# Kernel optimization log

Hardware: AMD Instinct MI355X
Metric: run time of the kernel (lower is better)

Reference implementation:

```python
import jax, jax.numpy as jnp
import numpy as np

N = 50000
E = 800000
D_IN = 128
D_H = 128
N_CLASSES = 40
N_HIDDEN = 2


def _gcn_norm(edge_index, num_nodes):
    # Add self loops, compute symmetric normalization D^-1/2 (A+I) D^-1/2
    loops = jnp.arange(num_nodes, dtype=edge_index.dtype)
    src = jnp.concatenate([edge_index[0], loops])
    dst = jnp.concatenate([edge_index[1], loops])
    deg = jax.ops.segment_sum(jnp.ones_like(src, dtype=jnp.float32), dst,
                              num_segments=num_nodes)
    dinv = jnp.where(deg > 0, jax.lax.rsqrt(jnp.maximum(deg, 1.0)), 0.0)
    norm = dinv[src] * dinv[dst]  # [E+N]
    return src, dst, norm


def _gcn_conv(x, src, dst, norm, W, b):
    h = x @ W                          # [N, d_out] transform first (PyG order)
    msg = h[src] * norm[:, None]       # gather + scale, [E+N, d_out]
    out = jax.ops.segment_sum(msg, dst, num_segments=x.shape[0])
    return out + b


def setup_inputs() -> dict:
    key = jax.random.key(0)
    ks = jax.random.split(key, 8)
    x = jax.random.normal(ks[0], (N, D_IN), dtype=jnp.float32)
    edge_index = jax.random.randint(ks[1], (2, E), 0, N, dtype=jnp.int64)
    s = 1.0 / np.sqrt(D_IN)
    W1 = jax.random.uniform(ks[2], (D_IN, D_H), minval=-s, maxval=s, dtype=jnp.float32)
    b1 = jnp.zeros((D_H,), dtype=jnp.float32)
    sh = 1.0 / np.sqrt(D_H)
    Wh = jax.random.uniform(ks[3], (N_HIDDEN, D_H, D_H), minval=-sh, maxval=sh, dtype=jnp.float32)
    bh = jnp.zeros((N_HIDDEN, D_H), dtype=jnp.float32)
    Wf = jax.random.uniform(ks[4], (D_H, N_CLASSES), minval=-sh, maxval=sh, dtype=jnp.float32)
    bf = jnp.zeros((N_CLASSES,), dtype=jnp.float32)
    return {"x": x, "edge_index": edge_index, "W1": W1, "b1": b1,
            "Wh": Wh, "bh": bh, "Wf": Wf, "bf": bf}


def reference(x, edge_index, W1, b1, Wh, bh, Wf, bf):
    src, dst, norm = _gcn_norm(edge_index, x.shape[0])
    h = jax.nn.relu(_gcn_conv(x, src, dst, norm, W1, b1))
    for i in range(Wh.shape[0]):  # small fixed layer count
        h = jax.nn.relu(_gcn_conv(h, src, dst, norm, Wh[i], bh[i]))
    # extra relu in original forward is a no-op after relu above
    return h @ Wf + bf
```

## Files before the change

kernel.cpp:

```cpp
#include <hip/hip_runtime.h>

#define D 128
#define NC 40

typedef __attribute__((ext_vector_type(8))) short short8v;
typedef __attribute__((ext_vector_type(4))) float f32x4;

__device__ __forceinline__ unsigned short f2bf(float f) {
    unsigned u = __float_as_uint(f);
    u += 0x7fff + ((u >> 16) & 1);
    return (unsigned short)(u >> 16);
}
__device__ __forceinline__ float bf2f(unsigned short h) {
    return __uint_as_float(((unsigned)h) << 16);
}

__device__ __forceinline__ int load_idx(const int* ei, long long pos, int is64) {
    return is64 ? ei[pos * 2] : ei[pos];
}

__device__ __forceinline__ int detect64(const int* __restrict__ ei) {
    int lane = threadIdx.x & 63;
    int hi = ei[lane * 2 + 1];
    return __any(hi != 0) ? 0 : 1;
}


__global__ void count_convert_kernel(const int* __restrict__ ei, int* __restrict__ deg,
                                     int E, int EB,
                                     const float* __restrict__ W1, const float* __restrict__ Wh,
                                     const float* __restrict__ Wf,
                                     unsigned short* __restrict__ Wc1, unsigned short* __restrict__ Wch0,
                                     unsigned short* __restrict__ Wch1, unsigned short* __restrict__ Wcf) {
    if (blockIdx.x < EB) {
        int is64 = detect64(ei);
        int e = blockIdx.x * 256 + threadIdx.x;
        if (e < E) {
            int d = load_idx(ei, (long long)E + e, is64);
            atomicAdd(&deg[d], 1);
        }
    } else {
        int idx = (blockIdx.x - EB) * 256 + threadIdx.x;
        if (idx < 49152) {
            int which = idx >> 14;
            int j = idx & 16383;
            int nn = j >> 7, k = j & 127;
            const float* W = (which == 0) ? W1 : (which == 1) ? Wh : Wh + 16384;
            unsigned short* o = (which == 0) ? Wc1 : (which == 1) ? Wch0 : Wch1;
            float v = W[k * 128 + nn];
            unsigned short h = f2bf(v);
            o[j] = h;
            o[16384 + j] = f2bf(v - bf2f(h));
        } else if (idx < 49152 + 6144) {
            int j = idx - 49152;
            int nn = j >> 7, k = j & 127;
            float v = (nn < NC) ? Wf[k * NC + nn] : 0.f;
            unsigned short h = f2bf(v);
            Wcf[j] = h;
            Wcf[6144 + j] = f2bf(v - bf2f(h));
        }
    }
}

__global__ void scan1_kernel(const int* __restrict__ deg, int* __restrict__ bsum, int m) {
    int i = blockIdx.x * 512 + threadIdx.x;
    int v = (i < m) ? deg[i] : 0;
    #pragma unroll
    for (int off = 32; off; off >>= 1) v += __shfl_down(v, off, 64);
    __shared__ int ws[8];
    if ((threadIdx.x & 63) == 0) ws[threadIdx.x >> 6] = v;
    __syncthreads();
    if (threadIdx.x == 0) {
        int s = 0;
        #pragma unroll
        for (int j = 0; j < 8; ++j) s += ws[j];
        bsum[blockIdx.x] = s;
    }
}

__global__ void scan3_kernel(const int* __restrict__ deg, const int* __restrict__ bsum,
                             int* __restrict__ rowptr, int* __restrict__ fill,
                             float* __restrict__ dinv, int n, int E, int nb) {
    int t = threadIdx.x;
    int lane = t & 63, w = t >> 6;
    int pv = (t < nb && t < (int)blockIdx.x) ? bsum[t] : 0;
    int rs = pv;
    #pragma unroll
    for (int off = 32; off; off >>= 1) rs += __shfl_down(rs, off, 64);
    __shared__ int red[8];
    if (lane == 0) red[w] = rs;
    __syncthreads();
    int base = 0;
    #pragma unroll
    for (int j = 0; j < 8; ++j) base += red[j];
    __syncthreads();

    int i = blockIdx.x * 512 + t;
    int v = (i < n) ? deg[i] : 0;
    int s = v;
    #pragma unroll
    for (int off = 1; off < 64; off <<= 1) {
        int x = __shfl_up(s, off, 64);
        if (lane >= off) s += x;
    }
    __shared__ int wsum[8];
    if (lane == 63) wsum[w] = s;
    __syncthreads();
    int wbase = 0;
    #pragma unroll
    for (int j = 0; j < 8; ++j) if (j < w) wbase += wsum[j];
    int excl = base + wbase + s - v;
    if (i < n) {
        rowptr[i] = excl;
        fill[i]   = excl;
        dinv[i]   = rsqrtf((float)(v + 1));
    }
    if (i == 0) rowptr[n] = E;
}

__global__ void scatter_kernel(const int* __restrict__ ei, int* __restrict__ fill,
                               const float* __restrict__ dinv, int2* __restrict__ col2, int E) {
    int is64 = detect64(ei);
    int e = blockIdx.x * 256 + threadIdx.x;
    if (e >= E) return;
    int s = load_idx(ei, (long long)e, is64);
    int d = load_idx(ei, (long long)E + e, is64);
    int pos = atomicAdd(&fill[d], 1);
    col2[pos] = make_int2(s, __float_as_int(dinv[s]));
}

__launch_bounds__(512)
__global__ void fused_steal_kernel(const float4* __restrict__ h4,
                                   const unsigned short* __restrict__ Wcvt,
                                   const float* __restrict__ bias,
                                   const float* __restrict__ dinv,
                                   const int* __restrict__ rowptr, const int2* __restrict__ col2,
                                   float* __restrict__ out, int n) {
    __shared__ unsigned short Ah[32 * 128];
    __shared__ unsigned short Al[32 * 128];
    __shared__ int pnodes[32];
    __shared__ int cnt;
    int t = threadIdx.x;
    int wv = t >> 6, l = t & 63;
    int p = l >> 5, li = l & 31;
    if (t == 0) cnt = 8;
    __syncthreads();

    int base = blockIdx.x * 32;
    int pr = wv;
    while (pr < 16) {
        int row = 2 * pr + p;
        int node = base + row;
        int nd = (node < n) ? node : (n - 1);
        if (li == 0) pnodes[row] = (node < n) ? node : -1;
        float dn = dinv[nd];
        size_t rowbase = (size_t)nd * 32;
        float4 hv = h4[rowbase + li];
        float4 acc;
        acc.x = hv.x * dn; acc.y = hv.y * dn; acc.z = hv.z * dn; acc.w = hv.w * dn;
        int e = rowptr[nd], e1 = rowptr[nd + 1];
        for (; e + 8 <= e1; e += 8) {
            int2 c[8];
            #pragma unroll
            for (int q = 0; q < 8; ++q) c[q] = col2[e + q];
            float4 v[8];
            #pragma unroll
            for (int q = 0; q < 8; ++q) v[q] = h4[(size_t)c[q].x * 32 + li];
            #pragma unroll
            for (int q = 0; q < 8; ++q) {
                float ds = __int_as_float(c[q].y);
                acc.x += v[q].x * ds; acc.y += v[q].y * ds;
                acc.z += v[q].z * ds; acc.w += v[q].w * ds;
            }
        }
        for (; e + 4 <= e1; e += 4) {
            int2 c[4];
            #pragma unroll
            for (int q = 0; q < 4; ++q) c[q] = col2[e + q];
            float4 v[4];
            #pragma unroll
            for (int q = 0; q < 4; ++q) v[q] = h4[(size_t)c[q].x * 32 + li];
            #pragma unroll
            for (int q = 0; q < 4; ++q) {
                float ds = __int_as_float(c[q].y);
                acc.x += v[q].x * ds; acc.y += v[q].y * ds;
                acc.z += v[q].z * ds; acc.w += v[q].w * ds;
            }
        }
        for (; e < e1; ++e) {
            int2 c = col2[e];
            float ds = __int_as_float(c.y);
            float4 v = h4[(size_t)c.x * 32 + li];
            acc.x += v.x * ds; acc.y += v.y * ds; acc.z += v.z * ds; acc.w += v.w * ds;
        }
        acc.x *= dn; acc.y *= dn; acc.z *= dn; acc.w *= dn;

        ushort4 hi, lo;
        hi.x = f2bf(acc.x); lo.x = f2bf(acc.x - bf2f(hi.x));
        hi.y = f2bf(acc.y); lo.y = f2bf(acc.y - bf2f(hi.y));
        hi.z = f2bf(acc.z); lo.z = f2bf(acc.z - bf2f(hi.z));
        hi.w = f2bf(acc.w); lo.w = f2bf(acc.w - bf2f(hi.w));
        int off = (row << 8) + ((li << 3) ^ ((row & 7) << 4));
        *(ushort4*)((char*)Ah + off) = hi;
        *(ushort4*)((char*)Al + off) = lo;

        int nxt;
        if (l == 0) nxt = atomicAdd(&cnt, 1);
        nxt = __shfl(nxt, 0);
        pr = nxt;
    }
    __syncthreads();

    int lr = l & 15, lh = l >> 4;
    const unsigned short* Whi = Wcvt;
    const unsigned short* Wlo = Wcvt + 128 * 128;
    int col = wv * 16 + lr;
    short8v bh[4], bl[4];
    #pragma unroll
    for (int ks = 0; ks < 4; ++ks) {
        bh[ks] = *(const short8v*)&Whi[col * 128 + ks * 32 + lh * 8];
        bl[ks] = *(const short8v*)&Wlo[col * 128 + ks * 32 + lh * 8];
    }
    float bv = bias[col];
    #pragma unroll
    for (int rt = 0; rt < 2; ++rt) {
        f32x4 o = (f32x4){0.f, 0.f, 0.f, 0.f};
        #pragma unroll
        for (int ks = 0; ks < 4; ++ks) {
            int arow = rt * 16 + lr;
            int aoff = (arow << 8) + (((ks << 6) + (lh << 4)) ^ ((arow & 7) << 4));
            short8v ah = *(short8v*)((char*)Ah + aoff);
            short8v al = *(short8v*)((char*)Al + aoff);
            o = __builtin_amdgcn_mfma_f32_16x16x32_bf16(ah, bh[ks], o, 0, 0, 0);
            o = __builtin_amdgcn_mfma_f32_16x16x32_bf16(ah, bl[ks], o, 0, 0, 0);
            o = __builtin_amdgcn_mfma_f32_16x16x32_bf16(al, bh[ks], o, 0, 0, 0);
        }
        #pragma unroll
        for (int r = 0; r < 4; ++r) {
            int prow = pnodes[rt * 16 + lh * 4 + r];
            if (prow >= 0) out[(size_t)prow * 128 + col] = fmaxf(o[r] + bv, 0.f);
        }
    }
}

__launch_bounds__(256)
__global__ void final_mfma_kernel(const float* __restrict__ A, const unsigned short* __restrict__ Wcvt,
                                  const float* __restrict__ bf, float* __restrict__ C, int M) {
    __shared__ unsigned short Ah[64 * 128];
    __shared__ unsigned short Al[64 * 128];
    int t = threadIdx.x;
    int l = t & 63, w = t >> 6;
    int lr = l & 15, lh = l >> 4;

    const unsigned short* Whi = Wcvt;
    const unsigned short* Wlo = Wcvt + 48 * 128;
    short8v bhi[3][4], blo[3][4];
    #pragma unroll
    for (int nt = 0; nt < 3; ++nt) {
        int n = nt * 16 + lr;
        #pragma unroll
        for (int ks = 0; ks < 4; ++ks) {
            bhi[nt][ks] = *(const short8v*)&Whi[n * 128 + ks * 32 + lh * 8];
            blo[nt][ks] = *(const short8v*)&Wlo[n * 128 + ks * 32 + lh * 8];
        }
    }

    int row0 = blockIdx.x * 64;
    #pragma unroll
    for (int c = 0; c < 4; ++c) {
        int chunk = c * 256 + t;
        int r  = chunk >> 4;
        int kc = chunk & 15;
        int gr = row0 + r; if (gr >= M) gr = M - 1;
        float4 a0 = *(const float4*)&A[(size_t)gr * 128 + kc * 8];
        float4 a1 = *(const float4*)&A[(size_t)gr * 128 + kc * 8 + 4];
        float av[8] = {a0.x, a0.y, a0.z, a0.w, a1.x, a1.y, a1.z, a1.w};
        short8v hv, lv;
        #pragma unroll
        for (int j = 0; j < 8; ++j) {
            unsigned short hi = f2bf(av[j]);
            hv[j] = (short)hi;
            lv[j] = (short)f2bf(av[j] - bf2f(hi));
        }
        int off = (r << 8) + ((kc << 4) ^ ((r & 7) << 4));
        *(short8v*)((char*)Ah + off) = hv;
        *(short8v*)((char*)Al + off) = lv;
    }
    __syncthreads();

    f32x4 acc[3];
    #pragma unroll
    for (int nt = 0; nt < 3; ++nt) acc[nt] = (f32x4){0.f, 0.f, 0.f, 0.f};
    int row = w * 16 + lr;
    #pragma unroll
    for (int ks = 0; ks < 4; ++ks) {
        int off = (row << 8) + (((ks << 6) + (lh << 4)) ^ ((row & 7) << 4));
        short8v ah = *(short8v*)((char*)Ah + off);
        short8v al = *(short8v*)((char*)Al + off);
        #pragma unroll
        for (int nt = 0; nt < 3; ++nt) {
            acc[nt] = __builtin_amdgcn_mfma_f32_16x16x32_bf16(ah, bhi[nt][ks], acc[nt], 0, 0, 0);
            acc[nt] = __builtin_amdgcn_mfma_f32_16x16x32_bf16(ah, blo[nt][ks], acc[nt], 0, 0, 0);
            acc[nt] = __builtin_amdgcn_mfma_f32_16x16x32_bf16(al, bhi[nt][ks], acc[nt], 0, 0, 0);
        }
    }
    #pragma unroll
    for (int nt = 0; nt < 3; ++nt) {
        int col = nt * 16 + lr;
        #pragma unroll
        for (int r = 0; r < 4; ++r) {
            int ro = row0 + w * 16 + lh * 4 + r;
            if (col < NC && ro < M) C[(size_t)ro * NC + col] = acc[nt][r] + bf[col];
        }
    }
}

extern "C" void kernel_launch(void* const* d_in, const int* in_sizes, int n_in,
                              void* d_out, int out_size, void* d_ws, size_t ws_size,
                              hipStream_t stream) {
    const float* x  = (const float*)d_in[0];
    const int*   ei = (const int*)d_in[1];
    const float* W1 = (const float*)d_in[2];
    const float* b1 = (const float*)d_in[3];
    const float* Wh = (const float*)d_in[4];
    const float* bh = (const float*)d_in[5];
    const float* Wf = (const float*)d_in[6];
    const float* bf = (const float*)d_in[7];
    float* out = (float*)d_out;

    int n = in_sizes[0] / D;
    int E = in_sizes[1] / 2;

    char* ws = (char*)d_ws;
    size_t off = 0;
    auto alloc = [&](size_t bytes) {
        void* p = ws + off;
        off = (off + bytes + 255) & ~(size_t)255;
        return p;
    };
    float* B0     = (float*)alloc((size_t)n * D * 4);
    float* B1     = (float*)alloc((size_t)n * D * 4);
    int*   deg    = (int*)alloc((size_t)n * 4);
    int*   rowptr = (int*)alloc((size_t)(n + 1) * 4);
    int*   fill   = (int*)alloc((size_t)n * 4);
    int2*  col2   = (int2*)alloc((size_t)E * 8);
    float* dinv   = (float*)alloc((size_t)n * 4);
    int*   bsum   = (int*)alloc(1024 * 4);
    unsigned short* Wc1  = (unsigned short*)alloc(2 * 128 * 128 * 2);
    unsigned short* Wch0 = (unsigned short*)alloc(2 * 128 * 128 * 2);
    unsigned short* Wch1 = (unsigned short*)alloc(2 * 128 * 128 * 2);
    unsigned short* Wcf  = (unsigned short*)alloc(2 * 48 * 128 * 2);

    int EB = (E + 255) / 256;
    int CB = (49152 + 6144 + 255) / 256;
    int nb = (n + 511) / 512;

    hipMemsetAsync(deg, 0, (size_t)n * 4, stream);
    count_convert_kernel<<<EB + CB, 256, 0, stream>>>(ei, deg, E, EB, W1, Wh, Wf, Wc1, Wch0, Wch1, Wcf);
    scan1_kernel<<<nb, 512, 0, stream>>>(deg, bsum, n);
    scan3_kernel<<<nb, 512, 0, stream>>>(deg, bsum, rowptr, fill, dinv, n, E, nb);
    scatter_kernel<<<EB, 256, 0, stream>>>(ei, fill, dinv, col2, E);

    int fgrid = (n + 31) / 32;

    fused_steal_kernel<<<fgrid, 512, 0, stream>>>((const float4*)x, Wc1, b1, dinv, rowptr, col2, B0, n);
    fused_steal_kernel<<<fgrid, 512, 0, stream>>>((const float4*)B0, Wch0, bh, dinv, rowptr, col2, B1, n);
    fused_steal_kernel<<<fgrid, 512, 0, stream>>>((const float4*)B1, Wch1, bh + D, dinv, rowptr, col2, B0, n);
    final_mfma_kernel<<<(n + 63) / 64, 256, 0, stream>>>(B0, Wcf, bf, out, n);
}
```

Measured before the change: 326.1 us.

## Fuse final classifier GEMM into last GCN layer and use half-wave node stealing

```diff
diff --git a/kernel.cpp b/kernel.cpp
--- a/kernel.cpp
+++ b/kernel.cpp
@@ -129,27 +129,42 @@
     col2[pos] = make_int2(s, __float_as_int(dinv[s]));
 }
 
+template<int FINAL>
 __launch_bounds__(512)
 __global__ void fused_steal_kernel(const float4* __restrict__ h4,
                                    const unsigned short* __restrict__ Wcvt,
                                    const float* __restrict__ bias,
                                    const float* __restrict__ dinv,
                                    const int* __restrict__ rowptr, const int2* __restrict__ col2,
-                                   float* __restrict__ out, int n) {
+                                   float* __restrict__ out,
+                                   const unsigned short* __restrict__ Wfc,
+                                   const float* __restrict__ bf,
+                                   float* __restrict__ outF, int n) {
     __shared__ unsigned short Ah[32 * 128];
     __shared__ unsigned short Al[32 * 128];
     __shared__ int pnodes[32];
     __shared__ int cnt;
     int t = threadIdx.x;
     int wv = t >> 6, l = t & 63;
-    int p = l >> 5, li = l & 31;
-    if (t == 0) cnt = 8;
-    __syncthreads();
+    int hp = l >> 5, li = l & 31;
+    int lr = l & 15, lh = l >> 4;
+    if (t == 0) cnt = 16;
+    __syncthreads();
+
+    const unsigned short* Whi = Wcvt;
+    const unsigned short* Wlo = Wcvt + 128 * 128;
+    int col = wv * 16 + lr;
+    short8v bh[4], bl[4];
+    #pragma unroll
+    for (int ks = 0; ks < 4; ++ks) {
+        bh[ks] = *(const short8v*)&Whi[col * 128 + ks * 32 + lh * 8];
+        bl[ks] = *(const short8v*)&Wlo[col * 128 + ks * 32 + lh * 8];
+    }
 
     int base = blockIdx.x * 32;
-    int pr = wv;
-    while (pr < 16) {
-        int row = 2 * pr + p;
+    int pr = wv * 2 + hp;
+    while (pr < 32) {
+        int row = pr;
         int node = base + row;
         int nd = (node < n) ? node : (n - 1);
         if (li == 0) pnodes[row] = (node < n) ? node : -1;
@@ -205,112 +220,83 @@
         *(ushort4*)((char*)Al + off) = lo;
 
         int nxt;
-        if (l == 0) nxt = atomicAdd(&cnt, 1);
-        nxt = __shfl(nxt, 0);
+        if (li == 0) nxt = atomicAdd(&cnt, 1);
+        nxt = __shfl(nxt, hp << 5);
         pr = nxt;
     }
     __syncthreads();
 
-    int lr = l & 15, lh = l >> 4;
-    const unsigned short* Whi = Wcvt;
-    const unsigned short* Wlo = Wcvt + 128 * 128;
-    int col = wv * 16 + lr;
-    short8v bh[4], bl[4];
-    #pragma unroll
-    for (int ks = 0; ks < 4; ++ks) {
-        bh[ks] = *(const short8v*)&Whi[col * 128 + ks * 32 + lh * 8];
-        bl[ks] = *(const short8v*)&Wlo[col * 128 + ks * 32 + lh * 8];
-    }
     float bv = bias[col];
+    f32x4 o[2];
     #pragma unroll
     for (int rt = 0; rt < 2; ++rt) {
-        f32x4 o = (f32x4){0.f, 0.f, 0.f, 0.f};
+        o[rt] = (f32x4){0.f, 0.f, 0.f, 0.f};
         #pragma unroll
         for (int ks = 0; ks < 4; ++ks) {
             int arow = rt * 16 + lr;
             int aoff = (arow << 8) + (((ks << 6) + (lh << 4)) ^ ((arow & 7) << 4));
             short8v ah = *(short8v*)((char*)Ah + aoff);
             short8v al = *(short8v*)((char*)Al + aoff);
-            o = __builtin_amdgcn_mfma_f32_16x16x32_bf16(ah, bh[ks], o, 0, 0, 0);
-            o = __builtin_amdgcn_mfma_f32_16x16x32_bf16(ah, bl[ks], o, 0, 0, 0);
-            o = __builtin_amdgcn_mfma_f32_16x16x32_bf16(al, bh[ks], o, 0, 0, 0);
-        }
+            o[rt] = __builtin_amdgcn_mfma_f32_16x16x32_bf16(ah, bh[ks], o[rt], 0, 0, 0);
+            o[rt] = __builtin_amdgcn_mfma_f32_16x16x32_bf16(ah, bl[ks], o[rt], 0, 0, 0);
+            o[rt] = __builtin_amdgcn_mfma_f32_16x16x32_bf16(al, bh[ks], o[rt], 0, 0, 0);
+        }
+    }
+
+    if constexpr (!FINAL) {
         #pragma unroll
-        for (int r = 0; r < 4; ++r) {
-            int prow = pnodes[rt * 16 + lh * 4 + r];
-            if (prow >= 0) out[(size_t)prow * 128 + col] = fmaxf(o[r] + bv, 0.f);
-        }
-    }
-}
-
-__launch_bounds__(256)
-__global__ void final_mfma_kernel(const float* __restrict__ A, const unsigned short* __restrict__ Wcvt,
-                                  const float* __restrict__ bf, float* __restrict__ C, int M) {
-    __shared__ unsigned short Ah[64 * 128];
-    __shared__ unsigned short Al[64 * 128];
-    int t = threadIdx.x;
-    int l = t & 63, w = t >> 6;
-    int lr = l & 15, lh = l >> 4;
-
-    const unsigned short* Whi = Wcvt;
-    const unsigned short* Wlo = Wcvt + 48 * 128;
-    short8v bhi[3][4], blo[3][4];
-    #pragma unroll
-    for (int nt = 0; nt < 3; ++nt) {
-        int n = nt * 16 + lr;
+        for (int rt = 0; rt < 2; ++rt) {
+            #pragma unroll
+            for (int r = 0; r < 4; ++r) {
+                int prow = pnodes[rt * 16 + lh * 4 + r];
+                if (prow >= 0) out[(size_t)prow * 128 + col] = fmaxf(o[rt][r] + bv, 0.f);
+            }
+        }
+    } else {
+        __syncthreads();
         #pragma unroll
-        for (int ks = 0; ks < 4; ++ks) {
-            bhi[nt][ks] = *(const short8v*)&Whi[n * 128 + ks * 32 + lh * 8];
-            blo[nt][ks] = *(const short8v*)&Wlo[n * 128 + ks * 32 + lh * 8];
-        }
-    }
-
-    int row0 = blockIdx.x * 64;
-    #pragma unroll
-    for (int c = 0; c < 4; ++c) {
-        int chunk = c * 256 + t;
-        int r  = chunk >> 4;
-        int kc = chunk & 15;
-        int gr = row0 + r; if (gr >= M) gr = M - 1;
-        float4 a0 = *(const float4*)&A[(size_t)gr * 128 + kc * 8];
-        float4 a1 = *(const float4*)&A[(size_t)gr * 128 + kc * 8 + 4];
-        float av[8] = {a0.x, a0.y, a0.z, a0.w, a1.x, a1.y, a1.z, a1.w};
-        short8v hv, lv;
-        #pragma unroll
-        for (int j = 0; j < 8; ++j) {
-            unsigned short hi = f2bf(av[j]);
-            hv[j] = (short)hi;
-            lv[j] = (short)f2bf(av[j] - bf2f(hi));
-        }
-        int off = (r << 8) + ((kc << 4) ^ ((r & 7) << 4));
-        *(short8v*)((char*)Ah + off) = hv;
-        *(short8v*)((char*)Al + off) = lv;
-    }
-    __syncthreads();
-
-    f32x4 acc[3];
-    #pragma unroll
-    for (int nt = 0; nt < 3; ++nt) acc[nt] = (f32x4){0.f, 0.f, 0.f, 0.f};
-    int row = w * 16 + lr;
-    #pragma unroll
-    for (int ks = 0; ks < 4; ++ks) {
-        int off = (row << 8) + (((ks << 6) + (lh << 4)) ^ ((row & 7) << 4));
-        short8v ah = *(short8v*)((char*)Ah + off);
-        short8v al = *(short8v*)((char*)Al + off);
-        #pragma unroll
-        for (int nt = 0; nt < 3; ++nt) {
-            acc[nt] = __builtin_amdgcn_mfma_f32_16x16x32_bf16(ah, bhi[nt][ks], acc[nt], 0, 0, 0);
-            acc[nt] = __builtin_amdgcn_mfma_f32_16x16x32_bf16(ah, blo[nt][ks], acc[nt], 0, 0, 0);
-            acc[nt] = __builtin_amdgcn_mfma_f32_16x16x32_bf16(al, bhi[nt][ks], acc[nt], 0, 0, 0);
-        }
-    }
-    #pragma unroll
-    for (int nt = 0; nt < 3; ++nt) {
-        int col = nt * 16 + lr;
-        #pragma unroll
-        for (int r = 0; r < 4; ++r) {
-            int ro = row0 + w * 16 + lh * 4 + r;
-            if (col < NC && ro < M) C[(size_t)ro * NC + col] = acc[nt][r] + bf[col];
+        for (int rt = 0; rt < 2; ++rt) {
+            #pragma unroll
+            for (int r = 0; r < 4; ++r) {
+                float v = fmaxf(o[rt][r] + bv, 0.f);
+                unsigned short hv = f2bf(v);
+                unsigned short lv = f2bf(v - bf2f(hv));
+                int row = rt * 16 + lh * 4 + r;
+                int boff = (row << 8) + ((2 * col) ^ ((row & 7) << 4));
+                *(unsigned short*)((char*)Ah + boff) = hv;
+                *(unsigned short*)((char*)Al + boff) = lv;
+            }
+        }
+        __syncthreads();
+        if (wv < 6) {
+            int rt = wv & 1, ct = wv >> 1;
+            int col48 = ct * 16 + lr;
+            const unsigned short* Fhi = Wfc;
+            const unsigned short* Flo = Wfc + 48 * 128;
+            short8v fh[4], fl[4];
+            #pragma unroll
+            for (int ks = 0; ks < 4; ++ks) {
+                fh[ks] = *(const short8v*)&Fhi[col48 * 128 + ks * 32 + lh * 8];
+                fl[ks] = *(const short8v*)&Flo[col48 * 128 + ks * 32 + lh * 8];
+            }
+            f32x4 of = (f32x4){0.f, 0.f, 0.f, 0.f};
+            #pragma unroll
+            for (int ks = 0; ks < 4; ++ks) {
+                int arow = rt * 16 + lr;
+                int aoff = (arow << 8) + (((ks << 6) + (lh << 4)) ^ ((arow & 7) << 4));
+                short8v ah = *(short8v*)((char*)Ah + aoff);
+                short8v al = *(short8v*)((char*)Al + aoff);
+                of = __builtin_amdgcn_mfma_f32_16x16x32_bf16(ah, fh[ks], of, 0, 0, 0);
+                of = __builtin_amdgcn_mfma_f32_16x16x32_bf16(ah, fl[ks], of, 0, 0, 0);
+                of = __builtin_amdgcn_mfma_f32_16x16x32_bf16(al, fh[ks], of, 0, 0, 0);
+            }
+            float bfv = (col48 < NC) ? bf[col48] : 0.f;
+            #pragma unroll
+            for (int r = 0; r < 4; ++r) {
+                int prow = pnodes[rt * 16 + lh * 4 + r];
+                if (prow >= 0 && col48 < NC)
+                    outF[(size_t)prow * NC + col48] = of[r] + bfv;
+            }
         }
     }
 }
@@ -363,8 +349,10 @@
 
     int fgrid = (n + 31) / 32;
 
-    fused_steal_kernel<<<fgrid, 512, 0, stream>>>((const float4*)x, Wc1, b1, dinv, rowptr, col2, B0, n);
-    fused_steal_kernel<<<fgrid, 512, 0, stream>>>((const float4*)B0, Wch0, bh, dinv, rowptr, col2, B1, n);
-    fused_steal_kernel<<<fgrid, 512, 0, stream>>>((const float4*)B1, Wch1, bh + D, dinv, rowptr, col2, B0, n);
-    final_mfma_kernel<<<(n + 63) / 64, 256, 0, stream>>>(B0, Wcf, bf, out, n);
-}
+    fused_steal_kernel<0><<<fgrid, 512, 0, stream>>>((const float4*)x, Wc1, b1, dinv, rowptr, col2,
+                                                     B0, Wcf, bf, out, n);
+    fused_steal_kernel<0><<<fgrid, 512, 0, stream>>>((const float4*)B0, Wch0, bh, dinv, rowptr, col2,
+                                                     B1, Wcf, bf, out, n);
+    fused_steal_kernel<1><<<fgrid, 512, 0, stream>>>((const float4*)B1, Wch1, bh + D, dinv, rowptr, col2,
+                                                     B0, Wcf, bf, out, n);
+}
```

Result: no change. 328.3 us (+0.7%).
